# Optimization experiments

Hardware: AMD Instinct MI355X
Metric: run time of the kernel (lower is better)

## Reference

```python
import jax, jax.numpy as jnp
import numpy as np

B, T, HID = 1, 256, 2048
H, D = 16, 128
KD = H * D
CONV = 4
MAX_CG = 30
LAMB_LB = 0.25
NORM_EPS = 1e-5


def setup_inputs() -> dict:
    key = jax.random.key(0)
    ks = jax.random.split(key, 10)
    s = 0.02
    init_lamb = float(np.log(np.exp(1.0 - LAMB_LB) - 1.0))  # softplus^-1(1 - lower_bound)
    return {
        "hidden_states": jax.random.normal(ks[0], (B, T, HID), jnp.float32),
        "Wq": jax.random.normal(ks[1], (HID, KD), jnp.float32) * s,
        "Wk": jax.random.normal(ks[2], (HID, KD), jnp.float32) * s,
        "Wv": jax.random.normal(ks[3], (HID, KD), jnp.float32) * s,
        "Wa": jax.random.normal(ks[4], (HID, H), jnp.float32) * s,
        "ba": jnp.full((H,), 2.0, jnp.float32),
        "Wb": jax.random.normal(ks[5], (HID, H), jnp.float32) * s,
        "bb": jnp.zeros((H,), jnp.float32),
        "conv_wq": jax.random.normal(ks[6], (KD, CONV), jnp.float32) * s,
        "conv_wk": jax.random.normal(ks[7], (KD, CONV), jnp.float32) * s,
        "lambda_params": jnp.full((KD,), init_lamb, jnp.float32),
        "o_norm_w": jnp.ones((D,), jnp.float32),
        "Wo": jax.random.normal(ks[8], (KD, HID), jnp.float32) * s,
    }


def short_conv_silu(x, w):
    # depthwise causal conv over time; x [b,t,c], w [c,k]
    k = w.shape[1]
    xp = jnp.pad(x, ((0, 0), (k - 1, 0), (0, 0)))
    t = x.shape[1]
    y = xp[:, 0:t, :] * w[:, 0]
    for i in range(1, k):
        y = y + xp[:, i:i + t, :] * w[:, i]
    return jax.nn.silu(y)


def l2norm(x):
    return x * jax.lax.rsqrt(jnp.sum(x * x, -1, keepdims=True) + 1e-6)


def rmsnorm(x, w):
    return x * jax.lax.rsqrt(jnp.mean(x * x, -1, keepdims=True) + NORM_EPS) * w


def cg_solve(A, b):
    # solve A x = b per (batch, head) with fixed CG iterations, x0 = 0
    matvec = lambda p: jnp.einsum('bhij,bhj->bhi', A, p)
    x0 = jnp.zeros_like(b)
    rs0 = jnp.sum(b * b, -1)

    def body(i, st):
        xc, r, p, rs = st
        Ap = matvec(p)
        alpha = rs / (jnp.sum(p * Ap, -1) + 1e-12)
        xc = xc + alpha[..., None] * p
        r = r - alpha[..., None] * Ap
        rs_n = jnp.sum(r * r, -1)
        p = r + (rs_n / (rs + 1e-12))[..., None] * p
        return xc, r, p, rs_n

    xf, _, _, _ = jax.lax.fori_loop(0, MAX_CG, body, (x0, b, b, rs0))
    return xf


def mesa_recurrence(q, k, v, g, beta, lamb_diag):
    # q,k,v [b,t,h,d]; g,beta [b,t,h]; lamb_diag [h,d,d]
    def step(carry, inp):
        h_kk, h_kv = carry
        qt, kt, vt, gt, bt = inp
        decay = jnp.exp(gt)[..., None, None]
        b_ = bt[..., None, None]
        h_kk = h_kk * decay + b_ * (kt[..., :, None] * kt[..., None, :])
        h_kv = h_kv * decay + b_ * (kt[..., :, None] * vt[..., None, :])
        A = h_kk + lamb_diag[None]
        q_star = cg_solve(A, qt)
        ot = jnp.einsum('bhk,bhkv->bhv', q_star, h_kv)
        return (h_kk, h_kv), ot

    init = (jnp.zeros((B, H, D, D), q.dtype), jnp.zeros((B, H, D, D), q.dtype))
    xs = (q.transpose(1, 0, 2, 3), k.transpose(1, 0, 2, 3), v.transpose(1, 0, 2, 3),
          g.transpose(1, 0, 2), beta.transpose(1, 0, 2))
    _, o = jax.lax.scan(step, init, xs)
    return o.transpose(1, 0, 2, 3)  # [b,t,h,d]


def reference(hidden_states, Wq, Wk, Wv, Wa, ba, Wb, bb, conv_wq, conv_wk,
              lambda_params, o_norm_w, Wo):
    x = hidden_states
    q = short_conv_silu(x @ Wq, conv_wq)
    k = short_conv_silu(x @ Wk, conv_wk)
    v = x @ Wv
    q = l2norm(q.reshape(B, T, H, D))
    k = l2norm(k.reshape(B, T, H, D))
    v = v.reshape(B, T, H, D)
    beta = jax.nn.sigmoid(x @ Wb + bb)          # [b,t,h]
    g = jax.nn.log_sigmoid(x @ Wa + ba)          # [b,t,h]
    lamb = (jax.nn.softplus(lambda_params) + LAMB_LB).reshape(H, D)
    lamb_diag = lamb[:, :, None] * jnp.eye(D, dtype=lamb.dtype)  # [h,d,d]
    o = mesa_recurrence(q, k, v, g, beta, lamb_diag)
    o = rmsnorm(o, o_norm_w)
    o = o.reshape(B, T, KD) @ Wo
    return o
```

## Files before the change

kernel.cpp:

```cpp
#include <hip/hip_runtime.h>
#include <math.h>

#define TT 256
#define HIDDEN 2048
#define NH 16
#define HD 128
#define KDIM 2048
#define NCG 30

typedef _Float16 h2 __attribute__((ext_vector_type(2)));
typedef _Float16 h4 __attribute__((ext_vector_type(4)));
typedef _Float16 half8 __attribute__((ext_vector_type(8)));
typedef float floatx4 __attribute__((ext_vector_type(4)));

__device__ __forceinline__ float wave_sum64(float v) {
#pragma unroll
    for (int off = 32; off > 0; off >>= 1) v += __shfl_xor(v, off, 64);
    return v;
}

__device__ __forceinline__ half8 cvt8(const float4 x, const float4 y) {
    half8 f;
    f[0] = (_Float16)x.x; f[1] = (_Float16)x.y; f[2] = (_Float16)x.z; f[3] = (_Float16)x.w;
    f[4] = (_Float16)y.x; f[5] = (_Float16)y.y; f[6] = (_Float16)y.z; f[7] = (_Float16)y.w;
    return f;
}

__device__ __forceinline__ void glds16(const void* g, void* l) {
    __builtin_amdgcn_global_load_lds(
        (const __attribute__((address_space(1))) void*)g,
        (__attribute__((address_space(3))) void*)l, 16, 0, 0);
}

__global__ __launch_bounds__(256) void wtrans_kernel(
    const float* __restrict__ W0, const float* __restrict__ W1,
    const float* __restrict__ W2, const float* __restrict__ W3,
    _Float16* __restrict__ T0, _Float16* __restrict__ T1,
    _Float16* __restrict__ T2, _Float16* __restrict__ T3)
{
    __shared__ float tile[64][68];
    const int z = blockIdx.z;
    const float* __restrict__ W = (z == 0) ? W0 : (z == 1) ? W1 : (z == 2) ? W2 : W3;
    _Float16* __restrict__ T = (z == 0) ? T0 : (z == 1) ? T1 : (z == 2) ? T2 : T3;
    const int k0 = blockIdx.x * 64, n0 = blockIdx.y * 64;
    const int tid = threadIdx.x;
#pragma unroll
    for (int p = 0; p < 4; p++) {
        const int idx = p * 256 + tid;
        const int r = idx >> 4, c = (idx & 15) * 4;
        const float4 v = *(const float4*)&W[(size_t)(k0 + r) * KDIM + n0 + c];
        tile[r][c] = v.x; tile[r][c + 1] = v.y; tile[r][c + 2] = v.z; tile[r][c + 3] = v.w;
    }
    __syncthreads();
#pragma unroll
    for (int p = 0; p < 2; p++) {
        const int c = p * 256 + tid;
        const int dn = c >> 3, c8 = c & 7;
        const int gk = k0 + c8 * 8, gn = n0 + dn;
        const int nt = gn >> 7, nn = gn & 127;
        const int kt = gk >> 5, kc = (gk >> 3) & 3;
        half8 o;
#pragma unroll
        for (int j = 0; j < 8; j++) o[j] = (_Float16)tile[c8 * 8 + j][dn];
        *(half8*)&T[(size_t)(((nt * 64 + kt) * 4 + kc)) * 1024 + nn * 8] = o;
    }
}

__global__ __launch_bounds__(256) void wab_trans_kernel(
    const float* __restrict__ Wa, const float* __restrict__ Wb, float* __restrict__ Tab)
{
    const int b = blockIdx.x;
    const int h = threadIdx.x & 15, kl = threadIdx.x >> 4;
    for (int p = 0; p < 16; p++) {
        const int k = b * 256 + p * 16 + kl;
        Tab[h * KDIM + k] = Wa[k * NH + h];
        Tab[(16 + h) * KDIM + k] = Wb[k * NH + h];
    }
}

#define ASTR 72
__global__ __launch_bounds__(256) void gemm_kernel(
    const float* __restrict__ A,
    const _Float16* __restrict__ Bb0, const _Float16* __restrict__ Bb1,
    const _Float16* __restrict__ Bb2,
    float* __restrict__ C0, float* __restrict__ C1, float* __restrict__ C2,
    int nTilesPerMat)
{
    __shared__ __align__(16) _Float16 Bsh[2][8192];
    __shared__ __align__(16) _Float16 Ash[2][32 * ASTR];

    const int tid = threadIdx.x, lane = tid & 63, w = tid >> 6;
    const int q = lane >> 4, l16 = lane & 15;
    const int nt = blockIdx.x, mt = blockIdx.y;
    const int mat = nt / nTilesPerMat;
    const int ntile = nt - mat * nTilesPerMat;
    const int n0 = ntile * 128;
    const _Float16* __restrict__ Bb = (mat == 0) ? Bb0 : (mat == 1) ? Bb1 : Bb2;
    float* __restrict__ C = (mat == 0) ? C0 : (mat == 1) ? C1 : C2;
    const int m0 = mt * 32;

    const _Float16* __restrict__ Btile = Bb + (size_t)ntile * 262144;
    const int ar = tid >> 3, ac = (tid & 7) * 8;
    const float* __restrict__ Ap = &A[(size_t)(m0 + ar) * KDIM + ac];

    floatx4 acc[2][2] = {};
    float4 ax, ay;

#pragma unroll
    for (int i = 0; i < 4; i++)
        glds16(Btile + (size_t)((w * 4 + i) * 64 + lane) * 8, &Bsh[0][(w * 4 + i) * 512]);
    ax = *(const float4*)&Ap[0]; ay = *(const float4*)&Ap[4];
    *(half8*)&Ash[0][ar * ASTR + ac] = cvt8(ax, ay);
    ax = *(const float4*)&Ap[64]; ay = *(const float4*)&Ap[68];
    __syncthreads();

    const int NSTEP = KDIM / 64;
    for (int s = 0; s < NSTEP; s++) {
        const int cur = s & 1;
        if (s + 1 < NSTEP) {
            const _Float16* src = Btile + (size_t)(s + 1) * 8192;
#pragma unroll
            for (int i = 0; i < 4; i++)
                glds16(src + (size_t)((w * 4 + i) * 64 + lane) * 8, &Bsh[cur ^ 1][(w * 4 + i) * 512]);
        }
#pragma unroll
        for (int kk = 0; kk < 2; kk++) {
            const half8 bf0 = *(const half8*)&Bsh[cur][kk * 4096 + q * 1024 + (w * 32 + l16) * 8];
            const half8 bf1 = *(const half8*)&Bsh[cur][kk * 4096 + q * 1024 + (w * 32 + 16 + l16) * 8];
            const half8 af0 = *(const half8*)&Ash[cur][l16 * ASTR + kk * 32 + q * 8];
            const half8 af1 = *(const half8*)&Ash[cur][(16 + l16) * ASTR + kk * 32 + q * 8];
            acc[0][0] = __builtin_amdgcn_mfma_f32_16x16x32_f16(af0, bf0, acc[0][0], 0, 0, 0);
            acc[0][1] = __builtin_amdgcn_mfma_f32_16x16x32_f16(af0, bf1, acc[0][1], 0, 0, 0);
            acc[1][0] = __builtin_amdgcn_mfma_f32_16x16x32_f16(af1, bf0, acc[1][0], 0, 0, 0);
            acc[1][1] = __builtin_amdgcn_mfma_f32_16x16x32_f16(af1, bf1, acc[1][1], 0, 0, 0);
        }
        if (s + 1 < NSTEP) {
            *(half8*)&Ash[cur ^ 1][ar * ASTR + ac] = cvt8(ax, ay);
            if (s + 2 < NSTEP) {
                ax = *(const float4*)&Ap[(s + 2) * 64];
                ay = *(const float4*)&Ap[(s + 2) * 64 + 4];
            }
        }
        __syncthreads();
    }

#pragma unroll
    for (int r = 0; r < 4; r++) {
        C[(size_t)(m0 + q * 4 + r) * KDIM + n0 + w * 32 + l16] = acc[0][0][r];
        C[(size_t)(m0 + q * 4 + r) * KDIM + n0 + w * 32 + 16 + l16] = acc[0][1][r];
        C[(size_t)(m0 + 16 + q * 4 + r) * KDIM + n0 + w * 32 + l16] = acc[1][0][r];
        C[(size_t)(m0 + 16 + q * 4 + r) * KDIM + n0 + w * 32 + 16 + l16] = acc[1][1][r];
    }
}

__global__ __launch_bounds__(256) void ab_kernel(
    const float* __restrict__ X, const float* __restrict__ Tab,
    const float* __restrict__ ba, const float* __restrict__ bb,
    float* __restrict__ g, float* __restrict__ beta)
{
    const int t = blockIdx.x;
    const int lane = threadIdx.x & 63, w = threadIdx.x >> 6;
    for (int oi = 0; oi < 8; oi++) {
        const int o = w * 8 + oi;
        const int h = o & 15, which = o >> 4;
        float acc = 0.f;
#pragma unroll
        for (int i = 0; i < 8; i++) {
            const int kk = lane * 4 + i * 256;
            const float4 xv = *(const float4*)&X[t * HIDDEN + kk];
            const float4 wv = *(const float4*)&Tab[o * KDIM + kk];
            acc = fmaf(xv.x, wv.x, acc); acc = fmaf(xv.y, wv.y, acc);
            acc = fmaf(xv.z, wv.z, acc); acc = fmaf(xv.w, wv.w, acc);
        }
        acc = wave_sum64(acc);
        if (lane == 0) {
            if (which == 0) {
                const float z = acc + ba[h];
                g[t * NH + h] = fminf(z, 0.f) - log1pf(__expf(-fabsf(z)));
            } else {
                const float z = acc + bb[h];
                beta[t * NH + h] = 1.f / (1.f + __expf(-z));
            }
        }
    }
}

__global__ __launch_bounds__(256) void prep_kernel(const float* __restrict__ g,
                                                   float* __restrict__ G,
                                                   const float* __restrict__ lp,
                                                   float* __restrict__ lamb)
{
    __shared__ float gs[TT * NH];
    const int tid = threadIdx.x;
    for (int i = tid; i < KDIM; i += 256) {
        const float x = lp[i];
        lamb[i] = fmaxf(x, 0.f) + log1pf(__expf(-fabsf(x))) + 0.25f;
    }
    for (int i = tid; i < TT * NH; i += 256) gs[i] = g[i];
    __syncthreads();
    if (tid < NH) {
        float run = 0.f;
        for (int t = 0; t < TT; t++) { run += gs[t * NH + tid]; gs[t * NH + tid] = run; }
    }
    __syncthreads();
    for (int i = tid; i < TT * NH; i += 256) G[i] = gs[i];
}

__global__ __launch_bounds__(256) void conv_silu_l2_kernel(
    const float* __restrict__ q_pre, const float* __restrict__ k_pre,
    const float* __restrict__ cwq, const float* __restrict__ cwk,
    float* __restrict__ qn, float* __restrict__ kn)
{
    const int t = blockIdx.x, h = blockIdx.y;
    const int which = threadIdx.x >> 7, d = threadIdx.x & 127;
    const int w = threadIdx.x >> 6;
    const int c = h * HD + d;
    const float* pre = which ? k_pre : q_pre;
    const float* cw  = which ? cwk : cwq;
    float y = 0.f;
#pragma unroll
    for (int i = 0; i < 4; i++) {
        const int ts = t - 3 + i;
        if (ts >= 0) y = fmaf(pre[ts * KDIM + c], cw[c * 4 + i], y);
    }
    const float s = y / (1.f + __expf(-y));
    float v = s * s;
#pragma unroll
    for (int off = 32; off > 0; off >>= 1) v += __shfl_down(v, off, 64);
    __shared__ float red[4];
    if ((threadIdx.x & 63) == 0) red[w] = v;
    __syncthreads();
    const float sum = red[which * 2] + red[which * 2 + 1];
    float* dst = which ? kn : qn;
    dst[t * KDIM + c] = s * rsqrtf(sum + 1e-6f);
}

#define PSTR 136
#define YSTR 264

template<int SMAX>
__device__ __forceinline__ void mesa_cg(
    const float* __restrict__ qn, const float* __restrict__ kn, const float* __restrict__ vv,
    const float* __restrict__ G, const float* __restrict__ bet, const float* __restrict__ lamb,
    const float* __restrict__ onw, float* __restrict__ out,
    int h, int t0, _Float16* Psh, _Float16* Ysh, float* red)
{
    constexpr int NSUB1 = SMAX / 64;
    constexpr int NK2   = SMAX / 32;

    const int tid = threadIdx.x, lane = tid & 63, w = tid >> 6;
    const int quad = lane >> 4, l16 = lane & 15;
    const int tmy = t0 + l16;
    const int dbase = w * 32;

    half8 K1[NSUB1][4];
#pragma unroll
    for (int ii = 0; ii < NSUB1; ii++) {
        const int srow = 16 * (w + 4 * ii) + l16;
        const float* kp = &kn[(srow * NH + h) * HD];
#pragma unroll
        for (int kk = 0; kk < 4; kk++) {
            const float4 a = *(const float4*)&kp[kk * 32 + quad * 8];
            const float4 b = *(const float4*)&kp[kk * 32 + quad * 8 + 4];
            K1[ii][kk] = cvt8(a, b);
        }
    }

    half8 KtF[2][NK2];
#pragma unroll
    for (int ss = 0; ss < 2; ss++) {
        const int d = dbase + ss * 16 + l16;
#pragma unroll
        for (int kk = 0; kk < NK2; kk++) {
#pragma unroll
            for (int j = 0; j < 8; j++) {
                const int s = kk * 32 + quad * 8 + j;
                KtF[ss][kk][j] = (_Float16)kn[(s * NH + h) * HD + d];
            }
        }
    }

    half8 Vf[NK2][2];
#pragma unroll
    for (int kk = 0; kk < NK2; kk++) {
#pragma unroll
        for (int ss = 0; ss < 2; ss++) {
            const int dv = dbase + ss * 16 + l16;
#pragma unroll
            for (int j = 0; j < 8; j++) {
                const int s = kk * 32 + quad * 8 + j;
                Vf[kk][ss][j] = (_Float16)vv[(s * NH + h) * HD + dv];
            }
        }
    }

    const float Gt = G[tmy * NH + h];
    float Wm[NSUB1][4];
#pragma unroll
    for (int ii = 0; ii < NSUB1; ii++)
#pragma unroll
        for (int r = 0; r < 4; r++) {
            const int s = 16 * (w + 4 * ii) + quad * 4 + r;
            Wm[ii][r] = (s <= tmy) ? bet[s * NH + h] * __expf(Gt - G[s * NH + h]) : 0.f;
        }
    float lam[8], xv[8], rv[8], pv[8];
#pragma unroll
    for (int ss = 0; ss < 2; ss++)
#pragma unroll
        for (int r = 0; r < 4; r++) {
            const int e = ss * 4 + r;
            const int d = dbase + ss * 16 + quad * 4 + r;
            lam[e] = lamb[h * HD + d];
            const float b = qn[(tmy * NH + h) * HD + d];
            xv[e] = 0.f; rv[e] = b; pv[e] = b;
        }
    float rs = 0.f;
#pragma unroll
    for (int e = 0; e < 8; e++) rs += rv[e] * rv[e];
    rs += __shfl_xor(rs, 16, 64); rs += __shfl_xor(rs, 32, 64);

    auto writeP = [&](const float* src) {
#pragma unroll
        for (int ss = 0; ss < 2; ss++) {
            h4 ph;
            ph.x = (_Float16)src[ss * 4 + 0]; ph.y = (_Float16)src[ss * 4 + 1];
            ph.z = (_Float16)src[ss * 4 + 2]; ph.w = (_Float16)src[ss * 4 + 3];
            *(h4*)&Psh[l16 * PSTR + dbase + ss * 16 + quad * 4] = ph;
        }
    };
    writeP(pv);

    for (int it = 0; it <= NCG; it++) {
        __syncthreads();
        floatx4 acc1a[NSUB1] = {}, acc1b[NSUB1] = {};
#pragma unroll
        for (int kk = 0; kk < 2; kk++) {
            const half8 bfa = *(const half8*)&Psh[l16 * PSTR + kk * 32 + quad * 8];
            const half8 bfb = *(const half8*)&Psh[l16 * PSTR + (kk + 2) * 32 + quad * 8];
#pragma unroll
            for (int ii = 0; ii < NSUB1; ii++) {
                acc1a[ii] = __builtin_amdgcn_mfma_f32_16x16x32_f16(K1[ii][kk], bfa, acc1a[ii], 0, 0, 0);
                acc1b[ii] = __builtin_amdgcn_mfma_f32_16x16x32_f16(K1[ii][kk + 2], bfb, acc1b[ii], 0, 0, 0);
            }
        }
#pragma unroll
        for (int ii = 0; ii < NSUB1; ii++) {
            h4 yh;
            yh.x = (_Float16)(Wm[ii][0] * (acc1a[ii][0] + acc1b[ii][0]));
            yh.y = (_Float16)(Wm[ii][1] * (acc1a[ii][1] + acc1b[ii][1]));
            yh.z = (_Float16)(Wm[ii][2] * (acc1a[ii][2] + acc1b[ii][2]));
            yh.w = (_Float16)(Wm[ii][3] * (acc1a[ii][3] + acc1b[ii][3]));
            *(h4*)&Ysh[l16 * YSTR + 16 * (w + 4 * ii) + quad * 4] = yh;
        }
        __syncthreads();
        if (it == NCG) break;

        floatx4 acc2a[2] = {}, acc2b[2] = {};
#pragma unroll
        for (int kk = 0; kk < NK2; kk += 2) {
            const half8 bf0 = *(const half8*)&Ysh[l16 * YSTR + kk * 32 + quad * 8];
            const half8 bf1 = *(const half8*)&Ysh[l16 * YSTR + (kk + 1) * 32 + quad * 8];
#pragma unroll
            for (int ss = 0; ss < 2; ss++) {
                acc2a[ss] = __builtin_amdgcn_mfma_f32_16x16x32_f16(KtF[ss][kk], bf0, acc2a[ss], 0, 0, 0);
                acc2b[ss] = __builtin_amdgcn_mfma_f32_16x16x32_f16(KtF[ss][kk + 1], bf1, acc2b[ss], 0, 0, 0);
            }
        }
        float Ap[8], pAp = 0.f;
#pragma unroll
        for (int ss = 0; ss < 2; ss++)
#pragma unroll
            for (int r = 0; r < 4; r++) {
                const int e = ss * 4 + r;
                Ap[e] = (acc2a[ss][r] + acc2b[ss][r]) + lam[e] * pv[e];
                pAp = fmaf(pv[e], Ap[e], pAp);
            }
        pAp += __shfl_xor(pAp, 16, 64); pAp += __shfl_xor(pAp, 32, 64);
        const float alpha = rs / (pAp + 1e-12f);
        float rsn = 0.f;
#pragma unroll
        for (int e = 0; e < 8; e++) {
            xv[e] = fmaf(alpha, pv[e], xv[e]);
            rv[e] = fmaf(-alpha, Ap[e], rv[e]);
            rsn = fmaf(rv[e], rv[e], rsn);
        }
        rsn += __shfl_xor(rsn, 16, 64); rsn += __shfl_xor(rsn, 32, 64);
        const float bcg = rsn / (rs + 1e-12f);
#pragma unroll
        for (int e = 0; e < 8; e++) pv[e] = fmaf(bcg, pv[e], rv[e]);
        rs = rsn;
        writeP(it == NCG - 1 ? xv : pv);
    }

    floatx4 accOa[2] = {}, accOb[2] = {};
#pragma unroll
    for (int kk = 0; kk < NK2; kk += 2) {
        const half8 af0 = *(const half8*)&Ysh[l16 * YSTR + kk * 32 + quad * 8];
        const half8 af1 = *(const half8*)&Ysh[l16 * YSTR + (kk + 1) * 32 + quad * 8];
#pragma unroll
        for (int ss = 0; ss < 2; ss++) {
            accOa[ss] = __builtin_amdgcn_mfma_f32_16x16x32_f16(af0, Vf[kk][ss], accOa[ss], 0, 0, 0);
            accOb[ss] = __builtin_amdgcn_mfma_f32_16x16x32_f16(af1, Vf[kk + 1][ss], accOb[ss], 0, 0, 0);
        }
    }
    float accO[2][4];
#pragma unroll
    for (int ss = 0; ss < 2; ss++)
#pragma unroll
        for (int r = 0; r < 4; r++) accO[ss][r] = accOa[ss][r] + accOb[ss][r];

    float part[4];
#pragma unroll
    for (int r = 0; r < 4; r++) {
        part[r] = accO[0][r] * accO[0][r] + accO[1][r] * accO[1][r];
#pragma unroll
        for (int off = 1; off < 16; off <<= 1) part[r] += __shfl_xor(part[r], off, 64);
    }
    if (l16 == 0) {
#pragma unroll
        for (int r = 0; r < 4; r++) red[w * 16 + quad * 4 + r] = part[r];
    }
    __syncthreads();
    const float w0 = onw[dbase + l16], w1 = onw[dbase + 16 + l16];
#pragma unroll
    for (int r = 0; r < 4; r++) {
        const int qr = quad * 4 + r;
        const float sumd = red[qr] + red[16 + qr] + red[32 + qr] + red[48 + qr];
        const float sc = rsqrtf(sumd * (1.f / HD) + 1e-5f);
        const int trow = ((t0 + qr) * NH + h) * HD;
        out[trow + dbase + l16] = accO[0][r] * sc * w0;
        out[trow + dbase + 16 + l16] = accO[1][r] * sc * w1;
    }
}

__global__ __launch_bounds__(256, 1) void mesa_kernel(
    const float* __restrict__ qn, const float* __restrict__ kn, const float* __restrict__ vv,
    const float* __restrict__ G, const float* __restrict__ bet, const float* __restrict__ lamb,
    const float* __restrict__ onw, float* __restrict__ out)
{
    __shared__ __align__(16) _Float16 Psh[16 * PSTR];
    __shared__ __align__(16) _Float16 Ysh[16 * YSTR];
    __shared__ float red[64];
    const int h = blockIdx.x, jb = blockIdx.y, t0 = jb * 16;
    switch (jb >> 2) {
        case 0:  mesa_cg<64> (qn, kn, vv, G, bet, lamb, onw, out, h, t0, Psh, Ysh, red); break;
        case 1:  mesa_cg<128>(qn, kn, vv, G, bet, lamb, onw, out, h, t0, Psh, Ysh, red); break;
        case 2:  mesa_cg<192>(qn, kn, vv, G, bet, lamb, onw, out, h, t0, Psh, Ysh, red); break;
        default: mesa_cg<256>(qn, kn, vv, G, bet, lamb, onw, out, h, t0, Psh, Ysh, red); break;
    }
}

extern "C" void kernel_launch(void* const* d_in, const int* in_sizes, int n_in,
                              void* d_out, int out_size, void* d_ws, size_t ws_size,
                              hipStream_t stream)
{
    (void)in_sizes; (void)n_in; (void)out_size; (void)ws_size;
    const float* x   = (const float*)d_in[0];
    const float* Wq  = (const float*)d_in[1];
    const float* Wk  = (const float*)d_in[2];
    const float* Wv  = (const float*)d_in[3];
    const float* Wa  = (const float*)d_in[4];
    const float* ba  = (const float*)d_in[5];
    const float* Wb  = (const float*)d_in[6];
    const float* bb  = (const float*)d_in[7];
    const float* cwq = (const float*)d_in[8];
    const float* cwk = (const float*)d_in[9];
    const float* lp  = (const float*)d_in[10];
    const float* onw = (const float*)d_in[11];
    const float* Wo  = (const float*)d_in[12];

    char* wsb = (char*)d_ws;
    float* q_pre = (float*)wsb;
    float* k_pre = q_pre + 524288;
    float* v     = k_pre + 524288;
    float* qn    = v + 524288;
    float* kn    = qn + 524288;
    float* g     = kn + 524288;
    float* beta  = g + 4096;
    float* G     = beta + 4096;
    float* lamb  = G + 4096;
    size_t off = ((size_t)((char*)(lamb + 2048) - wsb) + 1023) & ~(size_t)1023;
    _Float16* WtQ = (_Float16*)(wsb + off);
    _Float16* WtK = WtQ + (size_t)KDIM * KDIM;
    _Float16* WtV = WtK + (size_t)KDIM * KDIM;
    _Float16* WtO = WtV + (size_t)KDIM * KDIM;
    float* Tab    = (float*)(WtO + (size_t)KDIM * KDIM);
    float* onorm  = q_pre;
    float* outp   = (float*)d_out;

    wtrans_kernel<<<dim3(32, 32, 4), 256, 0, stream>>>(Wq, Wk, Wv, Wo, WtQ, WtK, WtV, WtO);
    wab_trans_kernel<<<8, 256, 0, stream>>>(Wa, Wb, Tab);

    gemm_kernel<<<dim3(48, 8), 256, 0, stream>>>(x, WtQ, WtK, WtV, q_pre, k_pre, v, 16);
    ab_kernel<<<dim3(TT), 256, 0, stream>>>(x, Tab, ba, bb, g, beta);
    prep_kernel<<<1, 256, 0, stream>>>(g, G, lp, lamb);
    conv_silu_l2_kernel<<<dim3(TT, NH), 256, 0, stream>>>(q_pre, k_pre, cwq, cwk, qn, kn);

    mesa_kernel<<<dim3(NH, 16), 256, 0, stream>>>(qn, kn, v, G, beta, lamb, onw, onorm);

    gemm_kernel<<<dim3(16, 8), 256, 0, stream>>>(onorm, WtO, WtO, WtO, outp, outp, outp, 16);
}
```

Before: 254.8 us.

## Fuse prep and Wa/Wb transpose kernels into neighbors, scan gates in mesa

Removes the single-block prep_kernel by computing the cumulative log-gate prefix sum per head inside each mesa block with a wave scan in shared memory, and computing softplus lambda inline. The Wa/Wb transpose is folded into wtrans_kernel as an extra z-slice, eliminating another launch. The transposed-weight store pattern is also remapped so consecutive threads write consecutive n columns. This saves launches and a serial single-thread scan, at the cost of redundant scans in every mesa block.

```diff
diff --git a/kernel.cpp b/kernel.cpp
--- a/kernel.cpp
+++ b/kernel.cpp
@@ -36,10 +36,24 @@
     const float* __restrict__ W0, const float* __restrict__ W1,
     const float* __restrict__ W2, const float* __restrict__ W3,
     _Float16* __restrict__ T0, _Float16* __restrict__ T1,
-    _Float16* __restrict__ T2, _Float16* __restrict__ T3)
-{
+    _Float16* __restrict__ T2, _Float16* __restrict__ T3,
+    const float* __restrict__ Wa, const float* __restrict__ Wb,
+    float* __restrict__ Tab)
+{
+    const int z = blockIdx.z;
+    if (z == 4) {
+        const int b = blockIdx.y * 32 + blockIdx.x;
+        if (b < 256) {
+            const int idx = b * 256 + threadIdx.x;
+            const int k = idx & 2047;
+            const int h = (idx >> 11) & 15;
+            const int which = idx >> 15;
+            const float* __restrict__ Wsrc = which ? Wb : Wa;
+            Tab[(which * 16 + h) * KDIM + k] = Wsrc[k * NH + h];
+        }
+        return;
+    }
     __shared__ float tile[64][68];
-    const int z = blockIdx.z;
     const float* __restrict__ W = (z == 0) ? W0 : (z == 1) ? W1 : (z == 2) ? W2 : W3;
     _Float16* __restrict__ T = (z == 0) ? T0 : (z == 1) ? T1 : (z == 2) ? T2 : T3;
     const int k0 = blockIdx.x * 64, n0 = blockIdx.y * 64;
@@ -54,27 +68,15 @@
     __syncthreads();
 #pragma unroll
     for (int p = 0; p < 2; p++) {
-        const int c = p * 256 + tid;
-        const int dn = c >> 3, c8 = c & 7;
-        const int gk = k0 + c8 * 8, gn = n0 + dn;
+        const int slot = p * 256 + tid;
+        const int ktc = slot >> 6, nn_loc = slot & 63;
+        const int gk = k0 + ktc * 8, gn = n0 + nn_loc;
         const int nt = gn >> 7, nn = gn & 127;
         const int kt = gk >> 5, kc = (gk >> 3) & 3;
         half8 o;
 #pragma unroll
-        for (int j = 0; j < 8; j++) o[j] = (_Float16)tile[c8 * 8 + j][dn];
+        for (int j = 0; j < 8; j++) o[j] = (_Float16)tile[ktc * 8 + j][nn_loc];
         *(half8*)&T[(size_t)(((nt * 64 + kt) * 4 + kc)) * 1024 + nn * 8] = o;
-    }
-}
-
-__global__ __launch_bounds__(256) void wab_trans_kernel(
-    const float* __restrict__ Wa, const float* __restrict__ Wb, float* __restrict__ Tab)
-{
-    const int b = blockIdx.x;
-    const int h = threadIdx.x & 15, kl = threadIdx.x >> 4;
-    for (int p = 0; p < 16; p++) {
-        const int k = b * 256 + p * 16 + kl;
-        Tab[h * KDIM + k] = Wa[k * NH + h];
-        Tab[(16 + h) * KDIM + k] = Wb[k * NH + h];
     }
 }
 
@@ -185,27 +187,6 @@
     }
 }
 
-__global__ __launch_bounds__(256) void prep_kernel(const float* __restrict__ g,
-                                                   float* __restrict__ G,
-                                                   const float* __restrict__ lp,
-                                                   float* __restrict__ lamb)
-{
-    __shared__ float gs[TT * NH];
-    const int tid = threadIdx.x;
-    for (int i = tid; i < KDIM; i += 256) {
-        const float x = lp[i];
-        lamb[i] = fmaxf(x, 0.f) + log1pf(__expf(-fabsf(x))) + 0.25f;
-    }
-    for (int i = tid; i < TT * NH; i += 256) gs[i] = g[i];
-    __syncthreads();
-    if (tid < NH) {
-        float run = 0.f;
-        for (int t = 0; t < TT; t++) { run += gs[t * NH + tid]; gs[t * NH + tid] = run; }
-    }
-    __syncthreads();
-    for (int i = tid; i < TT * NH; i += 256) G[i] = gs[i];
-}
-
 __global__ __launch_bounds__(256) void conv_silu_l2_kernel(
     const float* __restrict__ q_pre, const float* __restrict__ k_pre,
     const float* __restrict__ cwq, const float* __restrict__ cwk,
@@ -241,9 +222,10 @@
 template<int SMAX>
 __device__ __forceinline__ void mesa_cg(
     const float* __restrict__ qn, const float* __restrict__ kn, const float* __restrict__ vv,
-    const float* __restrict__ G, const float* __restrict__ bet, const float* __restrict__ lamb,
+    const float* __restrict__ g, const float* __restrict__ bet, const float* __restrict__ lp,
     const float* __restrict__ onw, float* __restrict__ out,
-    int h, int t0, _Float16* Psh, _Float16* Ysh, float* red)
+    int h, int t0, _Float16* Psh, _Float16* Ysh, float* red,
+    float* Gsh, float* bets)
 {
     constexpr int NSUB1 = SMAX / 64;
     constexpr int NK2   = SMAX / 32;
@@ -253,6 +235,22 @@
     const int tmy = t0 + l16;
     const int dbase = w * 32;
 
+    {
+        float sc = g[tid * NH + h];
+#pragma unroll
+        for (int off = 1; off < 64; off <<= 1) {
+            const float o = __shfl_up(sc, off, 64);
+            if (lane >= off) sc += o;
+        }
+        if (lane == 63) red[w] = sc;
+        bets[tid] = bet[tid * NH + h];
+        __syncthreads();
+        float woff = 0.f;
+        for (int u = 0; u < w; u++) woff += red[u];
+        Gsh[tid] = sc + woff;
+        __syncthreads();
+    }
+
     half8 K1[NSUB1][4];
 #pragma unroll
     for (int ii = 0; ii < NSUB1; ii++) {
@@ -294,14 +292,14 @@
         }
     }
 
-    const float Gt = G[tmy * NH + h];
+    const float Gt = Gsh[tmy];
     float Wm[NSUB1][4];
 #pragma unroll
     for (int ii = 0; ii < NSUB1; ii++)
 #pragma unroll
         for (int r = 0; r < 4; r++) {
             const int s = 16 * (w + 4 * ii) + quad * 4 + r;
-            Wm[ii][r] = (s <= tmy) ? bet[s * NH + h] * __expf(Gt - G[s * NH + h]) : 0.f;
+            Wm[ii][r] = (s <= tmy) ? bets[s] * __expf(Gt - Gsh[s]) : 0.f;
         }
     float lam[8], xv[8], rv[8], pv[8];
 #pragma unroll
@@ -310,7 +308,8 @@
         for (int r = 0; r < 4; r++) {
             const int e = ss * 4 + r;
             const int d = dbase + ss * 16 + quad * 4 + r;
-            lam[e] = lamb[h * HD + d];
+            const float lx = lp[h * HD + d];
+            lam[e] = fmaxf(lx, 0.f) + log1pf(__expf(-fabsf(lx))) + 0.25f;
             const float b = qn[(tmy * NH + h) * HD + d];
             xv[e] = 0.f; rv[e] = b; pv[e] = b;
         }
@@ -435,18 +434,20 @@
 
 __global__ __launch_bounds__(256, 1) void mesa_kernel(
     const float* __restrict__ qn, const float* __restrict__ kn, const float* __restrict__ vv,
-    const float* __restrict__ G, const float* __restrict__ bet, const float* __restrict__ lamb,
+    const float* __restrict__ g, const float* __restrict__ bet, const float* __restrict__ lp,
     const float* __restrict__ onw, float* __restrict__ out)
 {
     __shared__ __align__(16) _Float16 Psh[16 * PSTR];
     __shared__ __align__(16) _Float16 Ysh[16 * YSTR];
     __shared__ float red[64];
+    __shared__ float Gsh[256];
+    __shared__ float bets[256];
     const int h = blockIdx.x, jb = blockIdx.y, t0 = jb * 16;
     switch (jb >> 2) {
-        case 0:  mesa_cg<64> (qn, kn, vv, G, bet, lamb, onw, out, h, t0, Psh, Ysh, red); break;
-        case 1:  mesa_cg<128>(qn, kn, vv, G, bet, lamb, onw, out, h, t0, Psh, Ysh, red); break;
-        case 2:  mesa_cg<192>(qn, kn, vv, G, bet, lamb, onw, out, h, t0, Psh, Ysh, red); break;
-        default: mesa_cg<256>(qn, kn, vv, G, bet, lamb, onw, out, h, t0, Psh, Ysh, red); break;
+        case 0:  mesa_cg<64> (qn, kn, vv, g, bet, lp, onw, out, h, t0, Psh, Ysh, red, Gsh, bets); break;
+        case 1:  mesa_cg<128>(qn, kn, vv, g, bet, lp, onw, out, h, t0, Psh, Ysh, red, Gsh, bets); break;
+        case 2:  mesa_cg<192>(qn, kn, vv, g, bet, lp, onw, out, h, t0, Psh, Ysh, red, Gsh, bets); break;
+        default: mesa_cg<256>(qn, kn, vv, g, bet, lp, onw, out, h, t0, Psh, Ysh, red, Gsh, bets); break;
     }
 }
 
@@ -488,15 +489,14 @@
     float* onorm  = q_pre;
     float* outp   = (float*)d_out;
 
-    wtrans_kernel<<<dim3(32, 32, 4), 256, 0, stream>>>(Wq, Wk, Wv, Wo, WtQ, WtK, WtV, WtO);
-    wab_trans_kernel<<<8, 256, 0, stream>>>(Wa, Wb, Tab);
+    wtrans_kernel<<<dim3(32, 32, 5), 256, 0, stream>>>(Wq, Wk, Wv, Wo, WtQ, WtK, WtV, WtO,
+                                                       Wa, Wb, Tab);
 
     gemm_kernel<<<dim3(48, 8), 256, 0, stream>>>(x, WtQ, WtK, WtV, q_pre, k_pre, v, 16);
     ab_kernel<<<dim3(TT), 256, 0, stream>>>(x, Tab, ba, bb, g, beta);
-    prep_kernel<<<1, 256, 0, stream>>>(g, G, lp, lamb);
     conv_silu_l2_kernel<<<dim3(TT, NH), 256, 0, stream>>>(q_pre, k_pre, cwq, cwk, qn, kn);
 
-    mesa_kernel<<<dim3(NH, 16), 256, 0, stream>>>(qn, kn, v, G, beta, lamb, onw, onorm);
+    mesa_kernel<<<dim3(NH, 16), 256, 0, stream>>>(qn, kn, v, g, beta, lp, onw, onorm);
 
     gemm_kernel<<<dim3(16, 8), 256, 0, stream>>>(onorm, WtO, WtO, WtO, outp, outp, outp, 16);
 }
```

New measurement: 236.4 us. -7.2%, faster.
